# Performance work log

Measured on AMD Instinct MI355X. Metric: run time of the kernel, lower is better.

The kernel has to match this reference:

```python
import jax, jax.numpy as jnp
import numpy as np


def _rbf(X1, X2, log_ls):
    # exp(-||x1-x2||^2 / (2*ls^2)) via the squared-norm expansion
    sq1 = jnp.sum(X1 * X1, axis=-1)[:, None]
    sq2 = jnp.sum(X2 * X2, axis=-1)[None, :]
    d2 = jnp.maximum(sq1 + sq2 - 2.0 * (X1 @ X2.T), 0.0)
    ls2 = jnp.exp(2.0 * log_ls)
    return jnp.exp(-d2 / (2.0 * ls2))


def setup_inputs() -> dict:
    key = jax.random.key(0)
    k1, k2, k3 = jax.random.split(key, 3)
    N_way, K_shot, Q_query, D = 16, 32, 4096, 1024
    Zs = jax.random.normal(k1, (N_way * K_shot, D), dtype=jnp.float32)
    Ys = jax.random.randint(k2, (N_way * K_shot, 1), 0, N_way)
    Zq = jax.random.normal(k3, (N_way * Q_query, D), dtype=jnp.float32)
    log_ls = jnp.asarray(0.0, dtype=jnp.float32)
    log_noise = jnp.asarray(-3.0, dtype=jnp.float32)
    return {"Zs": Zs, "Ys": Ys, "Zq": Zq, "log_ls": log_ls,
            "log_noise": log_noise, "N_way": N_way}


def reference(Zs, Ys, Zq, log_ls, log_noise, N_way):
    Nsamp = Zs.shape[0]  # N_way * K_shot
    Y1hot = jax.nn.one_hot(Ys.reshape(-1), N_way, dtype=Zs.dtype)  # [Nsamp, N_way]
    noise = jnp.exp(2.0 * log_noise)
    Kss = _rbf(Zs, Zs, log_ls) + noise * jnp.eye(Nsamp, dtype=Zs.dtype)
    L = jnp.linalg.cholesky(Kss)
    alpha = jax.scipy.linalg.cho_solve((L, True), Y1hot)  # [Nsamp, N_way]
    Kqs = _rbf(Zq, Zs, log_ls)  # [Q, Nsamp]
    f_q = Kqs @ alpha  # [Q, N_way]
    return jax.nn.softmax(f_q, axis=-1)
```

## Files before the change

kernel.cpp:

```cpp
#include <hip/hip_runtime.h>
#include <math.h>

#define NS 512
#define NQ 65536
#define DD 1024
#define NW 16

typedef __attribute__((ext_vector_type(8))) short short8x;
typedef __attribute__((ext_vector_type(4))) float floatx4;

static __device__ __forceinline__ unsigned short bf_trunc(float x) {
  return (unsigned short)(__float_as_uint(x) >> 16);
}
static __device__ __forceinline__ float bf_tof(unsigned short h) {
  return __uint_as_float(((unsigned)h) << 16);
}
static __device__ __forceinline__ unsigned short bf_rne(float x) {
  unsigned u = __float_as_uint(x);
  return (unsigned short)((u + 0x7FFFu + ((u >> 16) & 1u)) >> 16);
}

#define STASH(Hp, Lp, row, k0, v) do {                                      \
    unsigned e_ = (unsigned)((((row) * 32 + (k0)) ^ (((row) & 7) << 3)));   \
    ushort4 h_, l_;                                                         \
    h_.x = bf_trunc((v).x); l_.x = bf_trunc((v).x - bf_tof(h_.x));          \
    h_.y = bf_trunc((v).y); l_.y = bf_trunc((v).y - bf_tof(h_.y));          \
    h_.z = bf_trunc((v).z); l_.z = bf_trunc((v).z - bf_tof(h_.z));          \
    h_.w = bf_trunc((v).w); l_.w = bf_trunc((v).w - bf_tof(h_.w));          \
    *(ushort4*)&Hp[e_] = h_; *(ushort4*)&Lp[e_] = l_;                       \
  } while (0)

__global__ void row_norms_kernel(const float* __restrict__ X, float* __restrict__ out, int nrows) {
  int gw = (int)((blockIdx.x * blockDim.x + threadIdx.x) >> 6);
  int lane = threadIdx.x & 63;
  if (gw >= nrows) return;
  const float* row = X + (size_t)gw * DD;
  float s = 0.f;
  #pragma unroll
  for (int i = 0; i < 4; ++i) {
    float4 v = *(const float4*)(row + 4 * lane + 256 * i);
    s += v.x * v.x + v.y * v.y + v.z * v.z + v.w * v.w;
  }
  #pragma unroll
  for (int off = 32; off; off >>= 1) s += __shfl_xor(s, off);
  if (lane == 0) out[gw] = s;
}

__global__ __launch_bounds__(256) void kss_kernel(const float* __restrict__ Zs,
                                                  const float* __restrict__ sn,
                                                  const float* __restrict__ log_ls,
                                                  const float* __restrict__ log_noise,
                                                  float* __restrict__ K) {
  __shared__ __align__(16) float At[16][68];
  __shared__ __align__(16) float Bt[16][68];
  int tid = threadIdx.x;
  int rb = blockIdx.y * 64, cb = blockIdx.x * 64;
  int tx = tid & 15, ty = tid >> 4;
  int srow = tid & 63, skq = (tid >> 6) << 2;
  float acc[4][4] = {};
  for (int kk = 0; kk < DD; kk += 16) {
    __syncthreads();
    float4 a = *(const float4*)(Zs + (size_t)(rb + srow) * DD + kk + skq);
    float4 b = *(const float4*)(Zs + (size_t)(cb + srow) * DD + kk + skq);
    At[skq + 0][srow] = a.x; At[skq + 1][srow] = a.y; At[skq + 2][srow] = a.z; At[skq + 3][srow] = a.w;
    Bt[skq + 0][srow] = b.x; Bt[skq + 1][srow] = b.y; Bt[skq + 2][srow] = b.z; Bt[skq + 3][srow] = b.w;
    __syncthreads();
    #pragma unroll
    for (int k = 0; k < 16; ++k) {
      float4 av = *(const float4*)&At[k][ty * 4];
      float4 bv = *(const float4*)&Bt[k][tx * 4];
      float aa[4] = {av.x, av.y, av.z, av.w};
      float bb[4] = {bv.x, bv.y, bv.z, bv.w};
      #pragma unroll
      for (int i = 0; i < 4; ++i)
        #pragma unroll
        for (int j = 0; j < 4; ++j)
          acc[i][j] = fmaf(aa[i], bb[j], acc[i][j]);
    }
  }
  float inv2 = 0.5f * expf(-2.f * log_ls[0]);
  float noise = expf(2.f * log_noise[0]);
  #pragma unroll
  for (int i = 0; i < 4; ++i)
    #pragma unroll
    for (int j = 0; j < 4; ++j) {
      int r = rb + ty * 4 + i, c = cb + tx * 4 + j;
      float d2 = fmaxf(sn[r] + sn[c] - 2.f * acc[i][j], 0.f);
      float v = expf(-d2 * inv2);
      if (r == c) v += noise;
      K[(size_t)r * NS + c] = v;
    }
}

__global__ __launch_bounds__(256) void panel_v2(float* __restrict__ K, int j) {
  __shared__ float Ld[64][68];
  __shared__ float idia_s[64];
  const int tid = threadIdx.x;

  if (tid < 64) {
    const int r = tid;
    float ar[64];
    #pragma unroll
    for (int c4 = 0; c4 < 16; ++c4)
      *(floatx4*)&ar[c4 * 4] = *(const floatx4*)(K + (size_t)(j + r) * NS + j + c4 * 4);
    float myinv = 0.f;
    #pragma unroll
    for (int c = 0; c < 64; ++c) {
      float colv = ar[c];
      float d = __shfl(colv, c);
      float sq = sqrtf(d);
      float inv = 1.f / sq;
      float x = (r > c) ? colv * inv : ((r == c) ? sq : 0.f);
      ar[c] = x;
      if (r == c) myinv = inv;
      #pragma unroll
      for (int k = c + 1; k < 64; ++k) {
        float xk = __shfl(x, k);
        ar[k] = fmaf(-x, xk, ar[k]);
      }
    }
    idia_s[r] = myinv;
    #pragma unroll
    for (int c4 = 0; c4 < 16; ++c4)
      *(floatx4*)&Ld[r][c4 * 4] = *(const floatx4*)&ar[c4 * 4];
    #pragma unroll
    for (int c = 0; c < 64; ++c) {
      if (c <= r) K[(size_t)(j + r) * NS + j + c] = ar[c];
      if (c < r)  K[(size_t)(j + c) * NS + j + r] = ar[c];
    }
  }
  __syncthreads();

  for (int r0 = j + 64 + tid; r0 < NS; r0 += 256) {
    float xr[64];
    #pragma unroll
    for (int c4 = 0; c4 < 16; ++c4)
      *(floatx4*)&xr[c4 * 4] = *(const floatx4*)(K + (size_t)r0 * NS + j + c4 * 4);
    #pragma unroll
    for (int g = 0; g < 16; ++g) {
      float v0 = xr[4 * g + 0], v1 = xr[4 * g + 1], v2 = xr[4 * g + 2], v3 = xr[4 * g + 3];
      for (int kb = 0; kb < g; ++kb) {
        floatx4 x4 = *(const floatx4*)&xr[4 * kb];
        floatx4 l0 = *(const floatx4*)&Ld[4 * g + 0][4 * kb];
        floatx4 l1 = *(const floatx4*)&Ld[4 * g + 1][4 * kb];
        floatx4 l2 = *(const floatx4*)&Ld[4 * g + 2][4 * kb];
        floatx4 l3 = *(const floatx4*)&Ld[4 * g + 3][4 * kb];
        v0 -= x4.x * l0.x + x4.y * l0.y + x4.z * l0.z + x4.w * l0.w;
        v1 -= x4.x * l1.x + x4.y * l1.y + x4.z * l1.z + x4.w * l1.w;
        v2 -= x4.x * l2.x + x4.y * l2.y + x4.z * l2.z + x4.w * l2.w;
        v3 -= x4.x * l3.x + x4.y * l3.y + x4.z * l3.z + x4.w * l3.w;
      }
      const int c0 = 4 * g;
      float x0 = v0 * idia_s[c0 + 0];
      v1 -= x0 * Ld[c0 + 1][c0];
      float x1 = v1 * idia_s[c0 + 1];
      v2 -= x0 * Ld[c0 + 2][c0] + x1 * Ld[c0 + 2][c0 + 1];
      float x2 = v2 * idia_s[c0 + 2];
      v3 -= x0 * Ld[c0 + 3][c0] + x1 * Ld[c0 + 3][c0 + 1] + x2 * Ld[c0 + 3][c0 + 2];
      float x3 = v3 * idia_s[c0 + 3];
      xr[c0 + 0] = x0; xr[c0 + 1] = x1; xr[c0 + 2] = x2; xr[c0 + 3] = x3;
    }
    #pragma unroll
    for (int c4 = 0; c4 < 16; ++c4)
      *(floatx4*)(K + (size_t)r0 * NS + j + c4 * 4) = *(const floatx4*)&xr[c4 * 4];
    #pragma unroll
    for (int c = 0; c < 64; ++c)
      K[(size_t)(j + c) * NS + r0] = xr[c];
  }
}

__global__ __launch_bounds__(256) void syrk_trailing(float* __restrict__ K, int j) {
  int t0 = j + 64;
  int rbt = t0 + blockIdx.y * 64, cbt = t0 + blockIdx.x * 64;
  if (cbt > rbt) return;
  __shared__ float A[64][69];
  __shared__ float B[64][69];
  int tid = threadIdx.x;
  for (int i = tid; i < 64 * 64; i += 256) {
    int r = i >> 6, k = i & 63;
    A[r][k] = K[(size_t)(rbt + r) * NS + j + k];
    B[r][k] = K[(size_t)(cbt + r) * NS + j + k];
  }
  __syncthreads();
  int tx = tid & 15, ty = tid >> 4;
  float acc[4][4] = {};
  for (int k = 0; k < 64; ++k) {
    float aa[4], bb[4];
    #pragma unroll
    for (int i = 0; i < 4; ++i) aa[i] = A[ty * 4 + i][k];
    #pragma unroll
    for (int i = 0; i < 4; ++i) bb[i] = B[tx * 4 + i][k];
    #pragma unroll
    for (int i = 0; i < 4; ++i)
      #pragma unroll
      for (int jj = 0; jj < 4; ++jj)
        acc[i][jj] = fmaf(aa[i], bb[jj], acc[i][jj]);
  }
  #pragma unroll
  for (int i = 0; i < 4; ++i)
    #pragma unroll
    for (int jj = 0; jj < 4; ++jj)
      K[(size_t)(rbt + ty * 4 + i) * NS + cbt + tx * 4 + jj] -= acc[i][jj];
}

__global__ __launch_bounds__(1024) void cho_solve_v2(const float* __restrict__ K,
                                                     const int* __restrict__ Ys,
                                                     unsigned short* __restrict__ alpha_t) {
  __shared__ float P[64][68];
  __shared__ float WsT[16][68];
  __shared__ float Wblk[64][16];
  __shared__ float invd[64];
  const int tid = threadIdx.x;
  const int rs = tid >> 4, nn = tid & 15;
  const int pc = nn * 4;

  float w[8];
  #pragma unroll
  for (int k = 0; k < 8; ++k) w[k] = (Ys[rs + 64 * k] == nn) ? 1.f : 0.f;

  for (int jb = 0; jb < 8; ++jb) {
    const int j = jb << 6;
    __syncthreads();
    #pragma unroll
    for (int k = 0; k < 8; ++k) if (k == jb) Wblk[rs][nn] = w[k];
    *(floatx4*)&P[rs][pc] = *(const floatx4*)(K + (size_t)(j + rs) * NS + j + pc);
    __syncthreads();
    if (tid < 64) {
      const int n = tid & 15, rq = tid >> 4;
      invd[tid] = 1.f / P[tid][tid];
      float w16[16];
      #pragma unroll
      for (int i = 0; i < 16; ++i) w16[i] = Wblk[rq + 4 * i][n];
      #pragma unroll
      for (int g = 0; g < 16; ++g) {
        floatx4 p[16];
        #pragma unroll
        for (int i = 0; i < 16; ++i) p[i] = *(const floatx4*)&P[rq + 4 * i][4 * g];
        #pragma unroll
        for (int cj = 0; cj < 4; ++cj) {
          const int c = 4 * g + cj;
          float xc = __shfl(w16[c >> 2], ((c & 3) << 4) + n) * invd[c];
          if (rq == (c & 3)) w16[c >> 2] = xc;
          #pragma unroll
          for (int i = 0; i < 16; ++i) {
            int r = rq + 4 * i;
            if (r > c) w16[i] -= p[i][cj] * xc;
          }
        }
      }
      #pragma unroll
      for (int i = 0; i < 16; ++i) WsT[n][rq + 4 * i] = w16[i];
    }
    __syncthreads();
    #pragma unroll
    for (int k = 0; k < 8; ++k) if (k == jb) w[k] = WsT[nn][rs];
    floatx4 wsr[16];
    #pragma unroll
    for (int g = 0; g < 16; ++g) wsr[g] = *(const floatx4*)&WsT[nn][4 * g];
    #pragma unroll
    for (int k = 0; k < 8; ++k) {
      if (k > jb) {
        const float* lrow = K + (size_t)(rs + 64 * k) * NS + j;
        float s = w[k];
        #pragma unroll
        for (int g = 0; g < 16; ++g) {
          floatx4 lv = *(const floatx4*)(lrow + 4 * g);
          s -= lv.x * wsr[g].x + lv.y * wsr[g].y + lv.z * wsr[g].z + lv.w * wsr[g].w;
        }
        w[k] = s;
      }
    }
  }

  for (int jb = 7; jb >= 0; --jb) {
    const int j = jb << 6;
    __syncthreads();
    #pragma unroll
    for (int k = 0; k < 8; ++k) if (k == jb) Wblk[rs][nn] = w[k];
    *(floatx4*)&P[rs][pc] = *(const floatx4*)(K + (size_t)(j + rs) * NS + j + pc);
    __syncthreads();
    if (tid < 64) {
      const int n = tid & 15, rq = tid >> 4;
      invd[tid] = 1.f / P[tid][tid];
      float w16[16];
      #pragma unroll
      for (int i = 0; i < 16; ++i) w16[i] = Wblk[rq + 4 * i][n];
      #pragma unroll
      for (int g = 15; g >= 0; --g) {
        floatx4 p[16];
        #pragma unroll
        for (int i = 0; i < 16; ++i) p[i] = *(const floatx4*)&P[rq + 4 * i][4 * g];
        #pragma unroll
        for (int cj = 3; cj >= 0; --cj) {
          const int c = 4 * g + cj;
          float xc = __shfl(w16[c >> 2], ((c & 3) << 4) + n) * invd[c];
          if (rq == (c & 3)) w16[c >> 2] = xc;
          #pragma unroll
          for (int i = 0; i < 16; ++i) {
            int r = rq + 4 * i;
            if (r < c) w16[i] -= p[i][cj] * xc;
          }
        }
      }
      #pragma unroll
      for (int i = 0; i < 16; ++i) WsT[n][rq + 4 * i] = w16[i];
    }
    __syncthreads();
    #pragma unroll
    for (int k = 0; k < 8; ++k) if (k == jb) w[k] = WsT[nn][rs];
    floatx4 wsr[16];
    #pragma unroll
    for (int g = 0; g < 16; ++g) wsr[g] = *(const floatx4*)&WsT[nn][4 * g];
    #pragma unroll
    for (int k = 0; k < 8; ++k) {
      if (k < jb) {
        const float* lrow = K + (size_t)(rs + 64 * k) * NS + j;
        float s = w[k];
        #pragma unroll
        for (int g = 0; g < 16; ++g) {
          floatx4 lv = *(const floatx4*)(lrow + 4 * g);
          s -= lv.x * wsr[g].x + lv.y * wsr[g].y + lv.z * wsr[g].z + lv.w * wsr[g].w;
        }
        w[k] = s;
      }
    }
  }

  #pragma unroll
  for (int k = 0; k < 8; ++k)
    alpha_t[(size_t)nn * NS + rs + 64 * k] = bf_rne(w[k]);
}

__global__ __launch_bounds__(512) void fused_v2(const float* __restrict__ Zq,
                                                const float* __restrict__ Zs,
                                                const float* __restrict__ sn,
                                                const unsigned short* __restrict__ alpha_t,
                                                const float* __restrict__ log_ls,
                                                float* __restrict__ out) {
  __shared__ __align__(16) unsigned short LB[32768];
  __shared__ float qnl[128];
  __shared__ float snl[256];
  unsigned short* AhB = LB;
  unsigned short* AlB = LB + 4096;
  unsigned short* BhB = LB + 8192;
  unsigned short* BlB = LB + 16384;
  unsigned short* KqB = LB;

  const int tid = threadIdx.x;
  const int lane = tid & 63;
  const int w = tid >> 6;
  const int wm = w >> 2, wn = w & 3;
  const int l15 = lane & 15, l4 = lane >> 4;
  const int rb = blockIdx.x * 128;
  const float inv2 = 0.5f * __expf(-2.f * log_ls[0]);
  const unsigned swz = (unsigned)((l15 & 7) << 3);

  if (tid < 128) qnl[tid] = 0.f;
  __syncthreads();

  const int qrow0 = tid >> 3;
  const int qk0 = (tid & 7) * 4;
  const int qrow1 = 64 + qrow0;

  floatx4 facc = {0.f, 0.f, 0.f, 0.f};

  for (int cc = 0; cc < NS; cc += 256) {
    if (tid < 256) snl[tid] = sn[cc + tid];
    floatx4 acc[4][4];
    #pragma unroll
    for (int a = 0; a < 4; ++a)
      #pragma unroll
      for (int b = 0; b < 4; ++b) acc[a][b] = (floatx4){0.f, 0.f, 0.f, 0.f};

    float4 pq0 = *(const float4*)(Zq + (size_t)(rb + qrow0) * DD + qk0);
    float4 pq1 = *(const float4*)(Zq + (size_t)(rb + qrow1) * DD + qk0);
    float4 ps[4];
    #pragma unroll
    for (int u = 0; u < 4; ++u) {
      int idx = tid + (u << 9);
      ps[u] = *(const float4*)(Zs + (size_t)(cc + (idx >> 3)) * DD + ((idx & 7) * 4));
    }

    for (int kt = 0; kt < 32; ++kt) {
      STASH(AhB, AlB, qrow0, qk0, pq0);
      STASH(AhB, AlB, qrow1, qk0, pq1);
      #pragma unroll
      for (int u = 0; u < 4; ++u) {
        int idx = tid + (u << 9);
        int srow = idx >> 3, sk0 = (idx & 7) * 4;
        STASH(BhB, BlB, srow, sk0, ps[u]);
      }
      if (cc == 0) {
        float s0 = pq0.x * pq0.x + pq0.y * pq0.y + pq0.z * pq0.z + pq0.w * pq0.w;
        float s1 = pq1.x * pq1.x + pq1.y * pq1.y + pq1.z * pq1.z + pq1.w * pq1.w;
        #pragma unroll
        for (int d = 1; d < 8; d <<= 1) { s0 += __shfl_xor(s0, d); s1 += __shfl_xor(s1, d); }
        if ((tid & 7) == 0) { qnl[qrow0] += s0; qnl[qrow1] += s1; }
      }
      __syncthreads();
      if (kt < 31) {
        int kk2 = (kt + 1) << 5;
        pq0 = *(const float4*)(Zq + (size_t)(rb + qrow0) * DD + kk2 + qk0);
        pq1 = *(const float4*)(Zq + (size_t)(rb + qrow1) * DD + kk2 + qk0);
        #pragma unroll
        for (int u = 0; u < 4; ++u) {
          int idx = tid + (u << 9);
          ps[u] = *(const float4*)(Zs + (size_t)(cc + (idx >> 3)) * DD + kk2 + ((idx & 7) * 4));
        }
      }
      short8x ah[4], al[4], bh[4], bl[4];
      #pragma unroll
      for (int mi = 0; mi < 4; ++mi) {
        unsigned e = (unsigned)((wm * 64 + mi * 16 + l15) * 32 + 8 * l4) ^ swz;
        ah[mi] = *(const short8x*)&AhB[e];
        al[mi] = *(const short8x*)&AlB[e];
      }
      #pragma unroll
      for (int ni = 0; ni < 4; ++ni) {
        unsigned e = (unsigned)((wn * 64 + ni * 16 + l15) * 32 + 8 * l4) ^ swz;
        bh[ni] = *(const short8x*)&BhB[e];
        bl[ni] = *(const short8x*)&BlB[e];
      }
      #pragma unroll
      for (int mi = 0; mi < 4; ++mi)
        #pragma unroll
        for (int ni = 0; ni < 4; ++ni) {
          acc[mi][ni] = __builtin_amdgcn_mfma_f32_16x16x32_bf16(ah[mi], bh[ni], acc[mi][ni], 0, 0, 0);
          acc[mi][ni] = __builtin_amdgcn_mfma_f32_16x16x32_bf16(ah[mi], bl[ni], acc[mi][ni], 0, 0, 0);
          acc[mi][ni] = __builtin_amdgcn_mfma_f32_16x16x32_bf16(al[mi], bh[ni], acc[mi][ni], 0, 0, 0);
        }
      __syncthreads();
    }

    short8x bfr[8];
    #pragma unroll
    for (int s = 0; s < 8; ++s)
      bfr[s] = *(const short8x*)(alpha_t + ((size_t)l15 * NS + cc + 32 * s + 8 * l4));

    #pragma unroll
    for (int mi = 0; mi < 4; ++mi)
      #pragma unroll
      for (int rr = 0; rr < 4; ++rr) {
        int row_l = wm * 64 + mi * 16 + l4 * 4 + rr;
        float qv = qnl[row_l];
        unsigned sw = (unsigned)((row_l & 7) << 3);
        #pragma unroll
        for (int ni = 0; ni < 4; ++ni) {
          int col = wn * 64 + ni * 16 + l15;
          float d2 = fmaxf(qv + snl[col] - 2.f * acc[mi][ni][rr], 0.f);
          float kq = __expf(-d2 * inv2);
          KqB[(unsigned)(row_l * 256 + col) ^ sw] = bf_rne(kq);
        }
      }
    __syncthreads();
    #pragma unroll
    for (int s = 0; s < 8; ++s) {
      unsigned e = (unsigned)((w * 16 + l15) * 256 + 32 * s + 8 * l4) ^ swz;
      short8x ak = *(const short8x*)&KqB[e];
      facc = __builtin_amdgcn_mfma_f32_16x16x32_bf16(ak, bfr[s], facc, 0, 0, 0);
    }
    __syncthreads();
  }

  #pragma unroll
  for (int r = 0; r < 4; ++r) {
    float v = facc[r];
    float m = v;
    #pragma unroll
    for (int d = 1; d < 16; d <<= 1) m = fmaxf(m, __shfl_xor(m, d));
    float e = __expf(v - m);
    float s = e;
    #pragma unroll
    for (int d = 1; d < 16; d <<= 1) s += __shfl_xor(s, d);
    out[(size_t)(rb + w * 16 + l4 * 4 + r) * NW + l15] = e / s;
  }
}

extern "C" void kernel_launch(void* const* d_in, const int* in_sizes, int n_in,
                              void* d_out, int out_size, void* d_ws, size_t ws_size,
                              hipStream_t stream) {
  (void)in_sizes; (void)n_in; (void)out_size; (void)ws_size;
  const float* Zs = (const float*)d_in[0];
  const int*   Ys = (const int*)d_in[1];
  const float* Zq = (const float*)d_in[2];
  const float* log_ls = (const float*)d_in[3];
  const float* log_noise = (const float*)d_in[4];
  float* out = (float*)d_out;

  float* ws = (float*)d_ws;
  float* K  = ws;
  float* sn = ws + (size_t)NS * NS;
  unsigned short* alpha_t = (unsigned short*)(sn + NS);

  row_norms_kernel<<<128, 256, 0, stream>>>(Zs, sn, NS);
  kss_kernel<<<dim3(8, 8), 256, 0, stream>>>(Zs, sn, log_ls, log_noise, K);
  for (int j = 0; j < NS; j += 64) {
    panel_v2<<<1, 256, 0, stream>>>(K, j);
    int rows = NS - j - 64;
    if (rows > 0) {
      int t = rows / 64;
      syrk_trailing<<<dim3(t, t), 256, 0, stream>>>(K, j);
    }
  }
  cho_solve_v2<<<1, 1024, 0, stream>>>(K, Ys, alpha_t);
  fused_v2<<<NQ / 128, 512, 0, stream>>>(Zq, Zs, sn, alpha_t, log_ls, out);
}
```

Baseline: 1.478 ms.

## Fuse Kss, blocked Cholesky and cho_solve into one persistent kernel with grid barriers

Replaces the chain of small launches (row norms, Kss, 8 panel + 7 syrk launches, and a single-block cho_solve) with one 36-workgroup persistent kernel that synchronises through an atomic grid barrier. It also fuses the diagonal-tile factorisation into the Kss/syrk step, spreads the panel TRSM rows across workgroups, and parallelises the triangular-solve updates across the grid. The aim is to remove launch overhead and the serial single-block stages that sit before the large fused query kernel. The cost is a spin-wait barrier that needs all 36 workgroups resident at once, plus a memset launch to reset the barrier counters.

```diff
diff --git a/kernel.cpp b/kernel.cpp
--- a/kernel.cpp
+++ b/kernel.cpp
@@ -5,6 +5,7 @@
 #define NQ 65536
 #define DD 1024
 #define NW 16
+#define NWG 36
 
 typedef __attribute__((ext_vector_type(8))) short short8x;
 typedef __attribute__((ext_vector_type(4))) float floatx4;
@@ -30,80 +31,32 @@
     *(ushort4*)&Hp[e_] = h_; *(ushort4*)&Lp[e_] = l_;                       \
   } while (0)
 
-__global__ void row_norms_kernel(const float* __restrict__ X, float* __restrict__ out, int nrows) {
-  int gw = (int)((blockIdx.x * blockDim.x + threadIdx.x) >> 6);
-  int lane = threadIdx.x & 63;
-  if (gw >= nrows) return;
-  const float* row = X + (size_t)gw * DD;
-  float s = 0.f;
-  #pragma unroll
-  for (int i = 0; i < 4; ++i) {
-    float4 v = *(const float4*)(row + 4 * lane + 256 * i);
-    s += v.x * v.x + v.y * v.y + v.z * v.z + v.w * v.w;
-  }
-  #pragma unroll
-  for (int off = 32; off; off >>= 1) s += __shfl_xor(s, off);
-  if (lane == 0) out[gw] = s;
-}
-
-__global__ __launch_bounds__(256) void kss_kernel(const float* __restrict__ Zs,
-                                                  const float* __restrict__ sn,
-                                                  const float* __restrict__ log_ls,
-                                                  const float* __restrict__ log_noise,
-                                                  float* __restrict__ K) {
-  __shared__ __align__(16) float At[16][68];
-  __shared__ __align__(16) float Bt[16][68];
-  int tid = threadIdx.x;
-  int rb = blockIdx.y * 64, cb = blockIdx.x * 64;
-  int tx = tid & 15, ty = tid >> 4;
-  int srow = tid & 63, skq = (tid >> 6) << 2;
-  float acc[4][4] = {};
-  for (int kk = 0; kk < DD; kk += 16) {
-    __syncthreads();
-    float4 a = *(const float4*)(Zs + (size_t)(rb + srow) * DD + kk + skq);
-    float4 b = *(const float4*)(Zs + (size_t)(cb + srow) * DD + kk + skq);
-    At[skq + 0][srow] = a.x; At[skq + 1][srow] = a.y; At[skq + 2][srow] = a.z; At[skq + 3][srow] = a.w;
-    Bt[skq + 0][srow] = b.x; Bt[skq + 1][srow] = b.y; Bt[skq + 2][srow] = b.z; Bt[skq + 3][srow] = b.w;
-    __syncthreads();
-    #pragma unroll
-    for (int k = 0; k < 16; ++k) {
-      float4 av = *(const float4*)&At[k][ty * 4];
-      float4 bv = *(const float4*)&Bt[k][tx * 4];
-      float aa[4] = {av.x, av.y, av.z, av.w};
-      float bb[4] = {bv.x, bv.y, bv.z, bv.w};
-      #pragma unroll
-      for (int i = 0; i < 4; ++i)
-        #pragma unroll
-        for (int j = 0; j < 4; ++j)
-          acc[i][j] = fmaf(aa[i], bb[j], acc[i][j]);
-    }
-  }
-  float inv2 = 0.5f * expf(-2.f * log_ls[0]);
-  float noise = expf(2.f * log_noise[0]);
-  #pragma unroll
-  for (int i = 0; i < 4; ++i)
-    #pragma unroll
-    for (int j = 0; j < 4; ++j) {
-      int r = rb + ty * 4 + i, c = cb + tx * 4 + j;
-      float d2 = fmaxf(sn[r] + sn[c] - 2.f * acc[i][j], 0.f);
-      float v = expf(-d2 * inv2);
-      if (r == c) v += noise;
-      K[(size_t)r * NS + c] = v;
-    }
-}
-
-__global__ __launch_bounds__(256) void panel_v2(float* __restrict__ K, int j) {
-  __shared__ float Ld[64][68];
-  __shared__ float idia_s[64];
+__device__ __forceinline__ void gbar(int* cnt, int* gen) {
+  __syncthreads();
+  if (threadIdx.x == 0) {
+    int g = __hip_atomic_load(gen, __ATOMIC_RELAXED, __HIP_MEMORY_SCOPE_AGENT);
+    __threadfence();
+    int p = __hip_atomic_fetch_add(cnt, 1, __ATOMIC_ACQ_REL, __HIP_MEMORY_SCOPE_AGENT);
+    if (p == NWG - 1) {
+      __hip_atomic_store(cnt, 0, __ATOMIC_RELAXED, __HIP_MEMORY_SCOPE_AGENT);
+      __hip_atomic_store(gen, g + 1, __ATOMIC_RELEASE, __HIP_MEMORY_SCOPE_AGENT);
+    } else {
+      while (__hip_atomic_load(gen, __ATOMIC_ACQUIRE, __HIP_MEMORY_SCOPE_AGENT) == g)
+        __builtin_amdgcn_s_sleep(2);
+    }
+    __threadfence();
+  }
+  __syncthreads();
+}
+
+__device__ __forceinline__ void potrf_tile(const float* T68, float* __restrict__ K, int j) {
   const int tid = threadIdx.x;
-
   if (tid < 64) {
     const int r = tid;
     float ar[64];
     #pragma unroll
     for (int c4 = 0; c4 < 16; ++c4)
-      *(floatx4*)&ar[c4 * 4] = *(const floatx4*)(K + (size_t)(j + r) * NS + j + c4 * 4);
-    float myinv = 0.f;
+      *(floatx4*)&ar[c4 * 4] = *(const floatx4*)&T68[r * 68 + c4 * 4];
     #pragma unroll
     for (int c = 0; c < 64; ++c) {
       float colv = ar[c];
@@ -112,223 +65,368 @@
       float inv = 1.f / sq;
       float x = (r > c) ? colv * inv : ((r == c) ? sq : 0.f);
       ar[c] = x;
-      if (r == c) myinv = inv;
       #pragma unroll
       for (int k = c + 1; k < 64; ++k) {
         float xk = __shfl(x, k);
         ar[k] = fmaf(-x, xk, ar[k]);
       }
     }
-    idia_s[r] = myinv;
-    #pragma unroll
-    for (int c4 = 0; c4 < 16; ++c4)
-      *(floatx4*)&Ld[r][c4 * 4] = *(const floatx4*)&ar[c4 * 4];
     #pragma unroll
     for (int c = 0; c < 64; ++c) {
       if (c <= r) K[(size_t)(j + r) * NS + j + c] = ar[c];
       if (c < r)  K[(size_t)(j + c) * NS + j + r] = ar[c];
     }
   }
-  __syncthreads();
-
-  for (int r0 = j + 64 + tid; r0 < NS; r0 += 256) {
-    float xr[64];
-    #pragma unroll
-    for (int c4 = 0; c4 < 16; ++c4)
-      *(floatx4*)&xr[c4 * 4] = *(const floatx4*)(K + (size_t)r0 * NS + j + c4 * 4);
+}
+
+__device__ __forceinline__ void solve_lower(const float* P, const float* invd,
+                                            const float* __restrict__ Wsrc16,
+                                            float* WsT, float* __restrict__ Wg, int j) {
+  const int tid = threadIdx.x;
+  if (tid < 64) {
+    const int n = tid & 15, rq = tid >> 4;
+    float w16[16];
+    #pragma unroll
+    for (int i = 0; i < 16; ++i) w16[i] = Wsrc16[(size_t)(rq + 4 * i) * 16 + n];
     #pragma unroll
     for (int g = 0; g < 16; ++g) {
-      float v0 = xr[4 * g + 0], v1 = xr[4 * g + 1], v2 = xr[4 * g + 2], v3 = xr[4 * g + 3];
-      for (int kb = 0; kb < g; ++kb) {
-        floatx4 x4 = *(const floatx4*)&xr[4 * kb];
-        floatx4 l0 = *(const floatx4*)&Ld[4 * g + 0][4 * kb];
-        floatx4 l1 = *(const floatx4*)&Ld[4 * g + 1][4 * kb];
-        floatx4 l2 = *(const floatx4*)&Ld[4 * g + 2][4 * kb];
-        floatx4 l3 = *(const floatx4*)&Ld[4 * g + 3][4 * kb];
-        v0 -= x4.x * l0.x + x4.y * l0.y + x4.z * l0.z + x4.w * l0.w;
-        v1 -= x4.x * l1.x + x4.y * l1.y + x4.z * l1.z + x4.w * l1.w;
-        v2 -= x4.x * l2.x + x4.y * l2.y + x4.z * l2.z + x4.w * l2.w;
-        v3 -= x4.x * l3.x + x4.y * l3.y + x4.z * l3.z + x4.w * l3.w;
-      }
-      const int c0 = 4 * g;
-      float x0 = v0 * idia_s[c0 + 0];
-      v1 -= x0 * Ld[c0 + 1][c0];
-      float x1 = v1 * idia_s[c0 + 1];
-      v2 -= x0 * Ld[c0 + 2][c0] + x1 * Ld[c0 + 2][c0 + 1];
-      float x2 = v2 * idia_s[c0 + 2];
-      v3 -= x0 * Ld[c0 + 3][c0] + x1 * Ld[c0 + 3][c0 + 1] + x2 * Ld[c0 + 3][c0 + 2];
-      float x3 = v3 * idia_s[c0 + 3];
-      xr[c0 + 0] = x0; xr[c0 + 1] = x1; xr[c0 + 2] = x2; xr[c0 + 3] = x3;
-    }
-    #pragma unroll
-    for (int c4 = 0; c4 < 16; ++c4)
-      *(floatx4*)(K + (size_t)r0 * NS + j + c4 * 4) = *(const floatx4*)&xr[c4 * 4];
-    #pragma unroll
-    for (int c = 0; c < 64; ++c)
-      K[(size_t)(j + c) * NS + r0] = xr[c];
-  }
-}
-
-__global__ __launch_bounds__(256) void syrk_trailing(float* __restrict__ K, int j) {
-  int t0 = j + 64;
-  int rbt = t0 + blockIdx.y * 64, cbt = t0 + blockIdx.x * 64;
-  if (cbt > rbt) return;
-  __shared__ float A[64][69];
-  __shared__ float B[64][69];
-  int tid = threadIdx.x;
-  for (int i = tid; i < 64 * 64; i += 256) {
-    int r = i >> 6, k = i & 63;
-    A[r][k] = K[(size_t)(rbt + r) * NS + j + k];
-    B[r][k] = K[(size_t)(cbt + r) * NS + j + k];
-  }
-  __syncthreads();
-  int tx = tid & 15, ty = tid >> 4;
-  float acc[4][4] = {};
-  for (int k = 0; k < 64; ++k) {
-    float aa[4], bb[4];
-    #pragma unroll
-    for (int i = 0; i < 4; ++i) aa[i] = A[ty * 4 + i][k];
-    #pragma unroll
-    for (int i = 0; i < 4; ++i) bb[i] = B[tx * 4 + i][k];
+      floatx4 p[16];
+      #pragma unroll
+      for (int i = 0; i < 16; ++i) p[i] = *(const floatx4*)&P[(rq + 4 * i) * 68 + 4 * g];
+      #pragma unroll
+      for (int cj = 0; cj < 4; ++cj) {
+        const int c = 4 * g + cj;
+        float xc = __shfl(w16[c >> 2], ((c & 3) << 4) + n) * invd[c];
+        if (rq == (c & 3)) w16[c >> 2] = xc;
+        #pragma unroll
+        for (int i = 0; i < 16; ++i) {
+          int r = rq + 4 * i;
+          if (r > c) w16[i] -= p[i][cj] * xc;
+        }
+      }
+    }
+    #pragma unroll
+    for (int i = 0; i < 16; ++i) {
+      WsT[n * 68 + rq + 4 * i] = w16[i];
+      Wg[(size_t)(j + rq + 4 * i) * 16 + n] = w16[i];
+    }
+  }
+}
+
+__device__ __forceinline__ void solve_upper(const float* P, const float* invd,
+                                            const float* __restrict__ Wsrc16,
+                                            float* __restrict__ Wg, int j) {
+  const int tid = threadIdx.x;
+  if (tid < 64) {
+    const int n = tid & 15, rq = tid >> 4;
+    float w16[16];
+    #pragma unroll
+    for (int i = 0; i < 16; ++i) w16[i] = Wsrc16[(size_t)(rq + 4 * i) * 16 + n];
+    #pragma unroll
+    for (int g = 15; g >= 0; --g) {
+      floatx4 p[16];
+      #pragma unroll
+      for (int i = 0; i < 16; ++i) p[i] = *(const floatx4*)&P[(rq + 4 * i) * 68 + 4 * g];
+      #pragma unroll
+      for (int cj = 3; cj >= 0; --cj) {
+        const int c = 4 * g + cj;
+        float xc = __shfl(w16[c >> 2], ((c & 3) << 4) + n) * invd[c];
+        if (rq == (c & 3)) w16[c >> 2] = xc;
+        #pragma unroll
+        for (int i = 0; i < 16; ++i) {
+          int r = rq + 4 * i;
+          if (r < c) w16[i] -= p[i][cj] * xc;
+        }
+      }
+    }
+    #pragma unroll
+    for (int i = 0; i < 16; ++i)
+      Wg[(size_t)(j + rq + 4 * i) * 16 + n] = w16[i];
+  }
+}
+
+__global__ __launch_bounds__(256) void setup_all(const float* __restrict__ Zs,
+                                                 const int* __restrict__ Ys,
+                                                 const float* __restrict__ log_ls,
+                                                 const float* __restrict__ log_noise,
+                                                 float* __restrict__ K,
+                                                 float* __restrict__ sn,
+                                                 float* __restrict__ Wg,
+                                                 unsigned short* __restrict__ alpha_t,
+                                                 int* cnt, int* gen) {
+  __shared__ float pf[13184];
+  const int wg = blockIdx.x, tid = threadIdx.x;
+
+  {
+    int wave = tid >> 6, lane = tid & 63;
+    for (int r = wg * 4 + wave; r < NS; r += NWG * 4) {
+      const float* row = Zs + (size_t)r * DD;
+      float s = 0.f;
+      #pragma unroll
+      for (int i = 0; i < 4; ++i) {
+        float4 v = *(const float4*)(row + 4 * lane + 256 * i);
+        s += v.x * v.x + v.y * v.y + v.z * v.z + v.w * v.w;
+      }
+      #pragma unroll
+      for (int off = 32; off; off >>= 1) s += __shfl_xor(s, off);
+      if (lane == 0) sn[r] = s;
+    }
+    int flat = wg * 256 + tid;
+    if (flat < NS * NW) Wg[flat] = (Ys[flat >> 4] == (flat & 15)) ? 1.f : 0.f;
+  }
+  gbar(cnt, gen);
+
+  {
+    int by = 0, accv = 0;
+    while (accv + by + 1 <= wg) { accv += by + 1; ++by; }
+    int bx = wg - accv;
+    const int rb = by * 64, cb = bx * 64;
+    float* At = pf;
+    float* Bt = pf + 1088;
+    float* Tile = pf + 8832;
+    const int tx = tid & 15, ty = tid >> 4;
+    const int srow = tid & 63, skq = (tid >> 6) << 2;
+    float acc[4][4] = {};
+    for (int kk = 0; kk < DD; kk += 16) {
+      __syncthreads();
+      float4 a = *(const float4*)(Zs + (size_t)(rb + srow) * DD + kk + skq);
+      float4 b = *(const float4*)(Zs + (size_t)(cb + srow) * DD + kk + skq);
+      At[(skq + 0) * 68 + srow] = a.x; At[(skq + 1) * 68 + srow] = a.y;
+      At[(skq + 2) * 68 + srow] = a.z; At[(skq + 3) * 68 + srow] = a.w;
+      Bt[(skq + 0) * 68 + srow] = b.x; Bt[(skq + 1) * 68 + srow] = b.y;
+      Bt[(skq + 2) * 68 + srow] = b.z; Bt[(skq + 3) * 68 + srow] = b.w;
+      __syncthreads();
+      #pragma unroll
+      for (int k = 0; k < 16; ++k) {
+        floatx4 av = *(const floatx4*)&At[k * 68 + ty * 4];
+        floatx4 bv = *(const floatx4*)&Bt[k * 68 + tx * 4];
+        #pragma unroll
+        for (int i = 0; i < 4; ++i)
+          #pragma unroll
+          for (int jj = 0; jj < 4; ++jj)
+            acc[i][jj] = fmaf(av[i], bv[jj], acc[i][jj]);
+      }
+    }
+    float inv2 = 0.5f * expf(-2.f * log_ls[0]);
+    float noise = expf(2.f * log_noise[0]);
     #pragma unroll
     for (int i = 0; i < 4; ++i)
       #pragma unroll
-      for (int jj = 0; jj < 4; ++jj)
-        acc[i][jj] = fmaf(aa[i], bb[jj], acc[i][jj]);
-  }
-  #pragma unroll
-  for (int i = 0; i < 4; ++i)
-    #pragma unroll
-    for (int jj = 0; jj < 4; ++jj)
-      K[(size_t)(rbt + ty * 4 + i) * NS + cbt + tx * 4 + jj] -= acc[i][jj];
-}
-
-__global__ __launch_bounds__(1024) void cho_solve_v2(const float* __restrict__ K,
-                                                     const int* __restrict__ Ys,
-                                                     unsigned short* __restrict__ alpha_t) {
-  __shared__ float P[64][68];
-  __shared__ float WsT[16][68];
-  __shared__ float Wblk[64][16];
-  __shared__ float invd[64];
-  const int tid = threadIdx.x;
-  const int rs = tid >> 4, nn = tid & 15;
-  const int pc = nn * 4;
-
-  float w[8];
-  #pragma unroll
-  for (int k = 0; k < 8; ++k) w[k] = (Ys[rs + 64 * k] == nn) ? 1.f : 0.f;
-
-  for (int jb = 0; jb < 8; ++jb) {
+      for (int jj = 0; jj < 4; ++jj) {
+        int r = rb + ty * 4 + i, c = cb + tx * 4 + jj;
+        float d2 = fmaxf(sn[r] + sn[c] - 2.f * acc[i][jj], 0.f);
+        float v = expf(-d2 * inv2);
+        if (r == c) v += noise;
+        K[(size_t)r * NS + c] = v;
+        if (wg == 0) Tile[(ty * 4 + i) * 68 + tx * 4 + jj] = v;
+      }
+    if (wg == 0) {
+      __syncthreads();
+      potrf_tile(Tile, K, 0);
+    }
+  }
+  gbar(cnt, gen);
+
+  for (int jb = 0; jb < 7; ++jb) {
     const int j = jb << 6;
-    __syncthreads();
-    #pragma unroll
-    for (int k = 0; k < 8; ++k) if (k == jb) Wblk[rs][nn] = w[k];
-    *(floatx4*)&P[rs][pc] = *(const floatx4*)(K + (size_t)(j + rs) * NS + j + pc);
-    __syncthreads();
-    if (tid < 64) {
-      const int n = tid & 15, rq = tid >> 4;
-      invd[tid] = 1.f / P[tid][tid];
-      float w16[16];
-      #pragma unroll
-      for (int i = 0; i < 16; ++i) w16[i] = Wblk[rq + 4 * i][n];
-      #pragma unroll
-      for (int g = 0; g < 16; ++g) {
-        floatx4 p[16];
-        #pragma unroll
-        for (int i = 0; i < 16; ++i) p[i] = *(const floatx4*)&P[rq + 4 * i][4 * g];
-        #pragma unroll
-        for (int cj = 0; cj < 4; ++cj) {
-          const int c = 4 * g + cj;
-          float xc = __shfl(w16[c >> 2], ((c & 3) << 4) + n) * invd[c];
-          if (rq == (c & 3)) w16[c >> 2] = xc;
+    {
+      float* Ld = pf;
+      float* invd = pf + 4416;
+      #pragma unroll
+      for (int it = 0; it < 4; ++it) {
+        int flat = tid + 256 * it;
+        int r = flat >> 4, c4 = (flat & 15) * 4;
+        *(floatx4*)&Ld[r * 68 + c4] = *(const floatx4*)&K[(size_t)(j + r) * NS + j + c4];
+      }
+      __syncthreads();
+      if (tid < 64) invd[tid] = 1.f / Ld[tid * 68 + tid];
+      __syncthreads();
+      const int r0 = j + 64 + wg + NWG * tid;
+      if (r0 < NS) {
+        float xr[64];
+        #pragma unroll
+        for (int c4 = 0; c4 < 16; ++c4)
+          *(floatx4*)&xr[c4 * 4] = *(const floatx4*)&K[(size_t)r0 * NS + j + c4 * 4];
+        #pragma unroll
+        for (int g = 0; g < 16; ++g) {
+          float v0 = xr[4 * g], v1 = xr[4 * g + 1], v2 = xr[4 * g + 2], v3 = xr[4 * g + 3];
+          for (int kb = 0; kb < g; ++kb) {
+            floatx4 x4 = *(const floatx4*)&xr[4 * kb];
+            floatx4 l0 = *(const floatx4*)&Ld[(4 * g + 0) * 68 + 4 * kb];
+            floatx4 l1 = *(const floatx4*)&Ld[(4 * g + 1) * 68 + 4 * kb];
+            floatx4 l2 = *(const floatx4*)&Ld[(4 * g + 2) * 68 + 4 * kb];
+            floatx4 l3 = *(const floatx4*)&Ld[(4 * g + 3) * 68 + 4 * kb];
+            v0 -= x4.x * l0.x + x4.y * l0.y + x4.z * l0.z + x4.w * l0.w;
+            v1 -= x4.x * l1.x + x4.y * l1.y + x4.z * l1.z + x4.w * l1.w;
+            v2 -= x4.x * l2.x + x4.y * l2.y + x4.z * l2.z + x4.w * l2.w;
+            v3 -= x4.x * l3.x + x4.y * l3.y + x4.z * l3.z + x4.w * l3.w;
+          }
+          const int c0 = 4 * g;
+          float x0 = v0 * invd[c0];
+          v1 -= x0 * Ld[(c0 + 1) * 68 + c0];
+          float x1 = v1 * invd[c0 + 1];
+          v2 -= x0 * Ld[(c0 + 2) * 68 + c0] + x1 * Ld[(c0 + 2) * 68 + c0 + 1];
+          float x2 = v2 * invd[c0 + 2];
+          v3 -= x0 * Ld[(c0 + 3) * 68 + c0] + x1 * Ld[(c0 + 3) * 68 + c0 + 1] + x2 * Ld[(c0 + 3) * 68 + c0 + 2];
+          float x3 = v3 * invd[c0 + 3];
+          xr[c0] = x0; xr[c0 + 1] = x1; xr[c0 + 2] = x2; xr[c0 + 3] = x3;
+        }
+        #pragma unroll
+        for (int c4 = 0; c4 < 16; ++c4)
+          *(floatx4*)(K + (size_t)r0 * NS + j + c4 * 4) = *(const floatx4*)&xr[c4 * 4];
+        #pragma unroll
+        for (int c = 0; c < 64; ++c)
+          K[(size_t)(j + c) * NS + r0] = xr[c];
+      }
+    }
+    gbar(cnt, gen);
+
+    {
+      const int T = 7 - jb;
+      const int nt = T * (T + 1) / 2;
+      if (wg < nt) {
+        int ti = 0, a2 = 0;
+        while (a2 + ti + 1 <= wg) { a2 += ti + 1; ++ti; }
+        int tj = wg - a2;
+        const int rbt = j + 64 + ti * 64, cbt = j + 64 + tj * 64;
+        float* A = pf;
+        float* B = pf + 4416;
+        float* Tile = pf + 8832;
+        for (int i = tid; i < 4096; i += 256) {
+          int r = i >> 6, k = i & 63;
+          A[r * 69 + k] = K[(size_t)(rbt + r) * NS + j + k];
+          B[r * 69 + k] = K[(size_t)(cbt + r) * NS + j + k];
+        }
+        __syncthreads();
+        const int tx = tid & 15, ty = tid >> 4;
+        float acc[4][4] = {};
+        for (int k = 0; k < 64; ++k) {
+          float aa[4], bb[4];
           #pragma unroll
-          for (int i = 0; i < 16; ++i) {
-            int r = rq + 4 * i;
-            if (r > c) w16[i] -= p[i][cj] * xc;
+          for (int i = 0; i < 4; ++i) aa[i] = A[(ty * 4 + i) * 69 + k];
+          #pragma unroll
+          for (int i = 0; i < 4; ++i) bb[i] = B[(tx * 4 + i) * 69 + k];
+          #pragma unroll
+          for (int i = 0; i < 4; ++i)
+            #pragma unroll
+            for (int jj = 0; jj < 4; ++jj)
+              acc[i][jj] = fmaf(aa[i], bb[jj], acc[i][jj]);
+        }
+        #pragma unroll
+        for (int i = 0; i < 4; ++i)
+          #pragma unroll
+          for (int jj = 0; jj < 4; ++jj) {
+            float* cp = &K[(size_t)(rbt + ty * 4 + i) * NS + cbt + tx * 4 + jj];
+            float nv = *cp - acc[i][jj];
+            *cp = nv;
+            if (wg == 0) Tile[(ty * 4 + i) * 68 + tx * 4 + jj] = nv;
           }
-        }
-      }
-      #pragma unroll
-      for (int i = 0; i < 16; ++i) WsT[n][rq + 4 * i] = w16[i];
-    }
-    __syncthreads();
-    #pragma unroll
-    for (int k = 0; k < 8; ++k) if (k == jb) w[k] = WsT[nn][rs];
-    floatx4 wsr[16];
-    #pragma unroll
-    for (int g = 0; g < 16; ++g) wsr[g] = *(const floatx4*)&WsT[nn][4 * g];
-    #pragma unroll
-    for (int k = 0; k < 8; ++k) {
-      if (k > jb) {
-        const float* lrow = K + (size_t)(rs + 64 * k) * NS + j;
-        float s = w[k];
+        if (wg == 0) {
+          __syncthreads();
+          potrf_tile(Tile, K, j + 64);
+        }
+      } else if (wg == 35) {
+        float* P = pf;
+        float* invd = pf + 4416;
+        float* WsT = pf + 5504;
+        #pragma unroll
+        for (int it = 0; it < 4; ++it) {
+          int flat = tid + 256 * it;
+          int r = flat >> 4, c4 = (flat & 15) * 4;
+          *(floatx4*)&P[r * 68 + c4] = *(const floatx4*)&K[(size_t)(j + r) * NS + j + c4];
+        }
+        __syncthreads();
+        if (tid < 64) invd[tid] = 1.f / P[tid * 68 + tid];
+        solve_lower(P, invd, Wg + (size_t)j * 16, WsT, Wg, j);
+        __syncthreads();
+        const int nrows = NS - j - 64;
+        for (int flat = tid; flat < nrows * 16; flat += 256) {
+          int row = j + 64 + (flat >> 4), nn = flat & 15;
+          float s = Wg[(size_t)row * 16 + nn];
+          const float* lrow = &K[(size_t)row * NS + j];
+          #pragma unroll
+          for (int g = 0; g < 16; ++g) {
+            floatx4 lv = *(const floatx4*)&lrow[4 * g];
+            floatx4 wv = *(const floatx4*)&WsT[nn * 68 + 4 * g];
+            s -= lv.x * wv.x + lv.y * wv.y + lv.z * wv.z + lv.w * wv.w;
+          }
+          Wg[(size_t)row * 16 + nn] = s;
+        }
+      }
+    }
+    gbar(cnt, gen);
+  }
+
+  {
+    const int j = 448;
+    if (wg == 35) {
+      float* P = pf;
+      float* invd = pf + 4416;
+      float* WsT = pf + 5504;
+      #pragma unroll
+      for (int it = 0; it < 4; ++it) {
+        int flat = tid + 256 * it;
+        int r = flat >> 4, c4 = (flat & 15) * 4;
+        *(floatx4*)&P[r * 68 + c4] = *(const floatx4*)&K[(size_t)(j + r) * NS + j + c4];
+      }
+      __syncthreads();
+      if (tid < 64) invd[tid] = 1.f / P[tid * 68 + tid];
+      solve_lower(P, invd, Wg + (size_t)j * 16, WsT, Wg, j);
+      solve_upper(P, invd, Wg + (size_t)j * 16, Wg, j);
+    }
+  }
+  gbar(cnt, gen);
+
+  for (int jb = 7; jb >= 1; --jb) {
+    const int j = jb << 6;
+    {
+      float* Wst = pf;
+      for (int e = tid; e < 1024; e += 256) {
+        int c = e >> 4, n = e & 15;
+        Wst[n * 68 + c] = Wg[(size_t)(j + c) * 16 + n];
+      }
+      __syncthreads();
+      const int row = wg + NWG * (tid >> 4);
+      const int nn = tid & 15;
+      if (row < j) {
+        float s = Wg[(size_t)row * 16 + nn];
+        const float* lrow = &K[(size_t)row * NS + j];
         #pragma unroll
         for (int g = 0; g < 16; ++g) {
-          floatx4 lv = *(const floatx4*)(lrow + 4 * g);
-          s -= lv.x * wsr[g].x + lv.y * wsr[g].y + lv.z * wsr[g].z + lv.w * wsr[g].w;
-        }
-        w[k] = s;
-      }
-    }
-  }
-
-  for (int jb = 7; jb >= 0; --jb) {
-    const int j = jb << 6;
-    __syncthreads();
-    #pragma unroll
-    for (int k = 0; k < 8; ++k) if (k == jb) Wblk[rs][nn] = w[k];
-    *(floatx4*)&P[rs][pc] = *(const floatx4*)(K + (size_t)(j + rs) * NS + j + pc);
-    __syncthreads();
-    if (tid < 64) {
-      const int n = tid & 15, rq = tid >> 4;
-      invd[tid] = 1.f / P[tid][tid];
-      float w16[16];
-      #pragma unroll
-      for (int i = 0; i < 16; ++i) w16[i] = Wblk[rq + 4 * i][n];
-      #pragma unroll
-      for (int g = 15; g >= 0; --g) {
-        floatx4 p[16];
-        #pragma unroll
-        for (int i = 0; i < 16; ++i) p[i] = *(const floatx4*)&P[rq + 4 * i][4 * g];
-        #pragma unroll
-        for (int cj = 3; cj >= 0; --cj) {
-          const int c = 4 * g + cj;
-          float xc = __shfl(w16[c >> 2], ((c & 3) << 4) + n) * invd[c];
-          if (rq == (c & 3)) w16[c >> 2] = xc;
-          #pragma unroll
-          for (int i = 0; i < 16; ++i) {
-            int r = rq + 4 * i;
-            if (r < c) w16[i] -= p[i][cj] * xc;
-          }
-        }
-      }
-      #pragma unroll
-      for (int i = 0; i < 16; ++i) WsT[n][rq + 4 * i] = w16[i];
-    }
-    __syncthreads();
-    #pragma unroll
-    for (int k = 0; k < 8; ++k) if (k == jb) w[k] = WsT[nn][rs];
-    floatx4 wsr[16];
-    #pragma unroll
-    for (int g = 0; g < 16; ++g) wsr[g] = *(const floatx4*)&WsT[nn][4 * g];
-    #pragma unroll
-    for (int k = 0; k < 8; ++k) {
-      if (k < jb) {
-        const float* lrow = K + (size_t)(rs + 64 * k) * NS + j;
-        float s = w[k];
-        #pragma unroll
-        for (int g = 0; g < 16; ++g) {
-          floatx4 lv = *(const floatx4*)(lrow + 4 * g);
-          s -= lv.x * wsr[g].x + lv.y * wsr[g].y + lv.z * wsr[g].z + lv.w * wsr[g].w;
-        }
-        w[k] = s;
-      }
-    }
-  }
-
-  #pragma unroll
-  for (int k = 0; k < 8; ++k)
-    alpha_t[(size_t)nn * NS + rs + 64 * k] = bf_rne(w[k]);
+          floatx4 lv = *(const floatx4*)&lrow[4 * g];
+          floatx4 wv = *(const floatx4*)&Wst[nn * 68 + 4 * g];
+          s -= lv.x * wv.x + lv.y * wv.y + lv.z * wv.z + lv.w * wv.w;
+        }
+        Wg[(size_t)row * 16 + nn] = s;
+      }
+    }
+    gbar(cnt, gen);
+    {
+      const int j2 = (jb - 1) << 6;
+      if (wg == 35) {
+        float* P = pf;
+        float* invd = pf + 4416;
+        #pragma unroll
+        for (int it = 0; it < 4; ++it) {
+          int flat = tid + 256 * it;
+          int r = flat >> 4, c4 = (flat & 15) * 4;
+          *(floatx4*)&P[r * 68 + c4] = *(const floatx4*)&K[(size_t)(j2 + r) * NS + j2 + c4];
+        }
+        __syncthreads();
+        if (tid < 64) invd[tid] = 1.f / P[tid * 68 + tid];
+        solve_upper(P, invd, Wg + (size_t)j2 * 16, Wg, j2);
+      }
+    }
+    gbar(cnt, gen);
+  }
+
+  {
+    int flat = wg * 256 + tid;
+    if (flat < NS * NW) {
+      int r = flat >> 4, nn = flat & 15;
+      alpha_t[(size_t)nn * NS + r] = bf_rne(Wg[(size_t)r * 16 + nn]);
+    }
+  }
 }
 
 __global__ __launch_bounds__(512) void fused_v2(const float* __restrict__ Zq,
@@ -491,17 +589,11 @@
   float* K  = ws;
   float* sn = ws + (size_t)NS * NS;
   unsigned short* alpha_t = (unsigned short*)(sn + NS);
-
-  row_norms_kernel<<<128, 256, 0, stream>>>(Zs, sn, NS);
-  kss_kernel<<<dim3(8, 8), 256, 0, stream>>>(Zs, sn, log_ls, log_noise, K);
-  for (int j = 0; j < NS; j += 64) {
-    panel_v2<<<1, 256, 0, stream>>>(K, j);
-    int rows = NS - j - 64;
-    if (rows > 0) {
-      int t = rows / 64;
-      syrk_trailing<<<dim3(t, t), 256, 0, stream>>>(K, j);
-    }
-  }
-  cho_solve_v2<<<1, 1024, 0, stream>>>(K, Ys, alpha_t);
+  float* Wg = sn + NS + 4096;
+  int* flags = (int*)(Wg + (size_t)NS * NW);
+
+  hipMemsetAsync(flags, 0, 2 * sizeof(int), stream);
+  setup_all<<<NWG, 256, 0, stream>>>(Zs, Ys, log_ls, log_noise, K, sn, Wg, alpha_t,
+                                     flags, flags + 1);
   fused_v2<<<NQ / 128, 512, 0, stream>>>(Zq, Zs, sn, alpha_t, log_ls, out);
 }
```

Result: slower. 2.370 ms (+60.4%).
